# Kernel tuning notes

Hardware: AMD Instinct MI355X
Metric: run time of the kernel (lower is better)

The kernel has to match this reference:

```python
import jax, jax.numpy as jnp
import numpy as np

B, S, NB = 2, 1024, 64
V, D, L, H, F = 1024, 512, 12, 8, 2048
DH = D // H
MAX_BARS = 256


def _ln(x, g, b):
    m = x.mean(-1, keepdims=True)
    v = ((x - m) ** 2).mean(-1, keepdims=True)
    return (x - m) * jax.lax.rsqrt(v + 1e-5) * g + b


def _rope(x, pos):
    # x: (B, T, H, DH), pos: (T,)
    half = x.shape[-1] // 2
    inv = 10000.0 ** (-jnp.arange(half, dtype=jnp.float32) / half)
    f = pos.astype(jnp.float32)[:, None] * inv  # (T, half)
    cos = jnp.cos(f)[None, :, None, :]
    sin = jnp.sin(f)[None, :, None, :]
    x1, x2 = x[..., :half], x[..., half:]
    return jnp.concatenate([x1 * cos - x2 * sin, x1 * sin + x2 * cos], -1)


def _swiglu(h, w1, w3, w2):
    return (jax.nn.silu(h @ w1) * (h @ w3)) @ w2


def _attention(sum_x, x, Wq, Wk, Wv, Wo, smask, umask, pos_s, pos_r):
    # shared QKV/O projections over both streams; 4-way block mask via concat keys
    b, nb, _ = sum_x.shape
    s = x.shape[1]

    def proj(t, W):
        return (t @ W).reshape(t.shape[0], t.shape[1], H, DH)

    qs = _rope(proj(sum_x, Wq), pos_s)
    qr = _rope(proj(x, Wq), pos_r)
    k = jnp.concatenate([_rope(proj(sum_x, Wk), pos_s), _rope(proj(x, Wk), pos_r)], 1)
    v = jnp.concatenate([proj(sum_x, Wv), proj(x, Wv)], 1)
    scale = DH ** -0.5

    def attend(q, mask):
        sc = jnp.einsum('bqhd,bkhd->bhqk', q, k) * scale
        sc = jnp.where(mask[:, None], sc, -1e9)
        p = jax.nn.softmax(sc, axis=-1)
        o = jnp.einsum('bhqk,bkhd->bqhd', p, v)
        return o.reshape(q.shape[0], q.shape[1], D)

    return attend(qs, smask) @ Wo, attend(qr, umask) @ Wo


def _forward(tok_emb, inst_emb, bar_emb,
             ln_as_g, ln_as_b, ln_ar_g, ln_ar_b,
             ln_fs_g, ln_fs_b, ln_fr_g, ln_fr_b,
             Wq, Wk, Wv, Wo,
             fs_w1, fs_w3, fs_w2, fr_w1, fr_w3, fr_w2,
             out_g, out_b,
             token_ids, chord_ids, instrument_ids, num_bars):
    b, s = token_ids.shape
    nb = num_bars
    x = tok_emb[token_ids] + inst_emb[jnp.clip(instrument_ids, 0, 129)]
    sum_x = jnp.broadcast_to(bar_emb[:nb][None], (b, nb, tok_emb.shape[1]))

    bars = jnp.arange(nb)
    idx = jnp.arange(s)
    # ss: summary b attends summaries b' <= b (causal over bars)
    ss = jnp.broadcast_to(jnp.tril(jnp.ones((nb, nb), bool))[None], (b, nb, nb))
    # sr: summary b summarizes regular tokens in bar b
    sr = chord_ids[:, None, :] == bars[None, :, None]  # (B, nb, S)
    smask = jnp.concatenate([ss, sr], -1)  # (B, nb, nb+S)
    # rs: regular i attends summaries of strictly previous bars
    rs = bars[None, None, :] < chord_ids[:, :, None]  # (B, S, nb)
    # rr: regular i attends regular j in same bar, causally
    rr = (chord_ids[:, :, None] == chord_ids[:, None, :]) & (idx[:, None] >= idx[None, :])
    umask = jnp.concatenate([rs, rr], -1)  # (B, S, nb+S)

    pos_s = jnp.arange(nb)
    pos_r = jnp.arange(s)

    for l in range(Wq.shape[0]):
        a_s, a_r = _attention(_ln(sum_x, ln_as_g[l], ln_as_b[l]),
                              _ln(x, ln_ar_g[l], ln_ar_b[l]),
                              Wq[l], Wk[l], Wv[l], Wo[l], smask, umask, pos_s, pos_r)
        sum_x = sum_x + a_s
        x = x + a_r
        sum_x = sum_x + _swiglu(_ln(sum_x, ln_fs_g[l], ln_fs_b[l]), fs_w1[l], fs_w3[l], fs_w2[l])
        x = x + _swiglu(_ln(x, ln_fr_g[l], ln_fr_b[l]), fr_w1[l], fr_w3[l], fr_w2[l])

    x = _ln(x, out_g, out_b)
    return x @ tok_emb.T  # tied lm_head


def setup_inputs():
    key = jax.random.key(0)
    it = iter(jax.random.split(key, 40))

    def nrm(shape):
        return jax.random.normal(next(it), shape, jnp.float32) * 0.02

    inp = {
        'token_ids': jax.random.randint(next(it), (B, S), 0, V),
        'chord_ids': jnp.sort(jax.random.randint(next(it), (B, S), 0, NB), axis=-1),
        'instrument_ids': jax.random.randint(next(it), (B, S), 0, 130),
        'num_bars': NB,
        'tok_emb': nrm((V, D)),
        'inst_emb': nrm((130, D)),
        'bar_emb': nrm((MAX_BARS, D)),
        'ln_as_g': jnp.ones((L, D)), 'ln_as_b': jnp.zeros((L, D)),
        'ln_ar_g': jnp.ones((L, D)), 'ln_ar_b': jnp.zeros((L, D)),
        'ln_fs_g': jnp.ones((L, D)), 'ln_fs_b': jnp.zeros((L, D)),
        'ln_fr_g': jnp.ones((L, D)), 'ln_fr_b': jnp.zeros((L, D)),
        'Wq': nrm((L, D, D)), 'Wk': nrm((L, D, D)),
        'Wv': nrm((L, D, D)), 'Wo': nrm((L, D, D)),
        'fs_w1': nrm((L, D, F)), 'fs_w3': nrm((L, D, F)), 'fs_w2': nrm((L, F, D)),
        'fr_w1': nrm((L, D, F)), 'fr_w3': nrm((L, D, F)), 'fr_w2': nrm((L, F, D)),
        'out_g': jnp.ones((D,)), 'out_b': jnp.zeros((D,)),
    }
    return inp


def reference(token_ids, chord_ids, instrument_ids, num_bars,
              tok_emb, inst_emb, bar_emb,
              ln_as_g, ln_as_b, ln_ar_g, ln_ar_b,
              ln_fs_g, ln_fs_b, ln_fr_g, ln_fr_b,
              Wq, Wk, Wv, Wo,
              fs_w1, fs_w3, fs_w2, fr_w1, fr_w3, fr_w2,
              out_g, out_b):
    return _forward(tok_emb, inst_emb, bar_emb,
                    ln_as_g, ln_as_b, ln_ar_g, ln_ar_b,
                    ln_fs_g, ln_fs_b, ln_fr_g, ln_fr_b,
                    Wq, Wk, Wv, Wo,
                    fs_w1, fs_w3, fs_w2, fr_w1, fr_w3, fr_w2,
                    out_g, out_b,
                    token_ids, chord_ids, instrument_ids, num_bars)
```

## Files before the change

### kernel.cpp

```cpp
#include <hip/hip_runtime.h>
#include <stdint.h>

#define NB 64
#define BATCH 2
#define SEQ 1024
#define DMODEL 512
#define NHEAD 8
#define DHEAD 64
#define FDIM 2048
#define NLAYER 12
#define VOCAB 1024
#define KTOT (NB + SEQ)
#define RSUM (BATCH * NB)
#define RREG (BATCH * SEQ)
#define RTOT (RSUM + RREG)

using bf16x8 = __attribute__((ext_vector_type(8))) short;
using f32x4  = __attribute__((ext_vector_type(4))) float;

__device__ __forceinline__ unsigned short f2bf(float f) {
  union { float f; unsigned u; } c; c.f = f;
  return (unsigned short)((c.u + 0x7fffu + ((c.u >> 16) & 1u)) >> 16);
}
__device__ __forceinline__ float bf2f(unsigned short s) {
  union { unsigned u; float f; } c; c.u = ((unsigned)s) << 16;
  return c.f;
}

template<int R>
__device__ __forceinline__ void stage_tile(
    const unsigned short* __restrict__ G, int K, int base_row, int k0,
    unsigned short (*lds)[64], int wid, int lane)
{
  const int rl = lane >> 3;
  const int j  = lane & 7;
  #pragma unroll
  for (int c = 0; c < R / 32; ++c) {
    const int r0 = wid * (R / 4) + c * 8;
    const int row = r0 + rl;
    const unsigned short* g = G + (size_t)(base_row + row) * K + k0
                                + ((j ^ (row & 7)) << 3);
    __builtin_amdgcn_global_load_lds(
        (const __attribute__((address_space(1))) void*)g,
        (__attribute__((address_space(3))) void*)&lds[r0][0], 16, 0, 0);
  }
}

__device__ __forceinline__ bf16x8 lds_frag(const unsigned short (*lds)[64],
                                           int row, int cc) {
  return *(const bf16x8*)&lds[row][(cc ^ (row & 7)) << 3];
}

template<int BM, int BN, int EPI>
__global__ __launch_bounds__(256) void gemm_bt(
    const unsigned short* __restrict__ A, const unsigned short* __restrict__ B0,
    const unsigned short* __restrict__ B1,
    void* __restrict__ Cout, const float* resid, int N, int K)
{
  constexpr int BK = 64;
  constexpr int WM = BM / 2, WN = BN / 2;
  constexpr int FM = WM / 16, FN = WN / 16;
  __shared__ __align__(16) unsigned short As[BM][BK];
  __shared__ __align__(16) unsigned short Bs[BN][BK];
  const int bm = blockIdx.y * BM, bn = blockIdx.x * BN;
  const unsigned short* __restrict__ BT = (bm < RSUM) ? B0 : B1;
  const int tid = threadIdx.x;
  const int wid = tid >> 6, lane = tid & 63;
  const int wm = wid >> 1, wn = wid & 1;
  const int lr = lane & 15, lk = lane >> 4;
  f32x4 acc[FM][FN] = {};
  for (int k0 = 0; k0 < K; k0 += BK) {
    __syncthreads();
    stage_tile<BM>(A,  K, bm, k0, As, wid, lane);
    stage_tile<BN>(BT, K, bn, k0, Bs, wid, lane);
    __syncthreads();
    #pragma unroll
    for (int kk = 0; kk < 2; ++kk) {
      bf16x8 af[FM], bfr[FN];
      #pragma unroll
      for (int m = 0; m < FM; ++m)
        af[m] = lds_frag(As, wm * WM + m * 16 + lr, kk * 4 + lk);
      #pragma unroll
      for (int n = 0; n < FN; ++n)
        bfr[n] = lds_frag(Bs, wn * WN + n * 16 + lr, kk * 4 + lk);
      #pragma unroll
      for (int m = 0; m < FM; ++m)
        #pragma unroll
        for (int n = 0; n < FN; ++n)
          acc[m][n] = __builtin_amdgcn_mfma_f32_16x16x32_bf16(af[m], bfr[n], acc[m][n], 0, 0, 0);
    }
  }
  #pragma unroll
  for (int m = 0; m < FM; ++m)
    #pragma unroll
    for (int n = 0; n < FN; ++n)
      #pragma unroll
      for (int i = 0; i < 4; ++i) {
        int row = bm + wm * WM + m * 16 + lk * 4 + i;
        int col = bn + wn * WN + n * 16 + lr;
        float v = acc[m][n][i];
        if constexpr (EPI == 1) {
          const float other = __shfl_xor(v, 1, 64);
          if (!(lr & 1)) {
            const float g = v, u = other;
            const float hv = (g / (1.f + __expf(-g))) * u;
            unsigned short* C = (unsigned short*)Cout;
            C[(size_t)row * (N >> 1) + (col >> 1)] = f2bf(hv);
          }
        } else if constexpr (EPI == 2) {
          unsigned short* C = (unsigned short*)Cout;
          C[(size_t)row * N + col] = f2bf(v);
        } else {
          float* C = (float*)Cout;
          size_t idx = (size_t)row * N + col;
          if (resid) v += resid[idx];
          C[idx] = v;
        }
      }
}

__global__ __launch_bounds__(256) void transpose_conv_kernel(
    const float* __restrict__ src, unsigned short* __restrict__ dst,
    int K, int N, size_t sstride, size_t dstride, int rmul, int radd)
{
  __shared__ float tile[32][33];
  const float* s = src + (size_t)blockIdx.z * sstride;
  unsigned short* d = dst + (size_t)blockIdx.z * dstride;
  const int k0 = blockIdx.y * 32, n0 = blockIdx.x * 32;
  const int tx = threadIdx.x & 31, ty = threadIdx.x >> 5;
  #pragma unroll
  for (int i = 0; i < 32; i += 8)
    tile[ty + i][tx] = s[(size_t)(k0 + ty + i) * N + n0 + tx];
  __syncthreads();
  #pragma unroll
  for (int i = 0; i < 32; i += 8)
    d[((size_t)(n0 + ty + i) * rmul + radd) * K + k0 + tx] = f2bf(tile[tx][ty + i]);
}

__global__ __launch_bounds__(256) void convert_bf16_kernel(
    const float* __restrict__ src, unsigned short* __restrict__ dst)
{
  const int i = (blockIdx.x * 256 + threadIdx.x) * 4;
  const float4 v = *(const float4*)&src[i];
  union { unsigned short u[4]; uint2 q; } o;
  o.u[0] = f2bf(v.x); o.u[1] = f2bf(v.y); o.u[2] = f2bf(v.z); o.u[3] = f2bf(v.w);
  *(uint2*)&dst[i] = o.q;
}

__global__ __launch_bounds__(128) void embed_kernel(
    const int* __restrict__ tok, const int* __restrict__ inst,
    const float* __restrict__ tok_emb, const float* __restrict__ inst_emb,
    const float* __restrict__ bar_emb, float* __restrict__ z)
{
  const int r = blockIdx.x, t = threadIdx.x;
  float4 val;
  if (r < RSUM) {
    const int bar = r & (NB - 1);
    val = *(const float4*)&bar_emb[(size_t)bar * DMODEL + t * 4];
  } else {
    const int rr = r - RSUM;
    const int b = rr >> 10, i = rr & (SEQ - 1);
    const int tk = tok[b * SEQ + i];
    int ins = inst[b * SEQ + i];
    ins = ins < 0 ? 0 : (ins > 129 ? 129 : ins);
    const float4 a = *(const float4*)&tok_emb[(size_t)tk * DMODEL + t * 4];
    const float4 cc = *(const float4*)&inst_emb[(size_t)ins * DMODEL + t * 4];
    val.x = a.x + cc.x; val.y = a.y + cc.y; val.z = a.z + cc.z; val.w = a.w + cc.w;
  }
  *(float4*)&z[(size_t)r * DMODEL + t * 4] = val;
}

__global__ __launch_bounds__(256) void ln_dual_kernel(
    const float* __restrict__ x, const float* __restrict__ g_s,
    const float* __restrict__ b_s, const float* __restrict__ g_r,
    const float* __restrict__ b_r, unsigned short* __restrict__ out)
{
  const int wid = threadIdx.x >> 6, lane = threadIdx.x & 63;
  const size_t row = (size_t)blockIdx.x * 4 + wid;
  const float* g = (row < RSUM) ? g_s : g_r;
  const float* bb = (row < RSUM) ? b_s : b_r;
  const float* xr = x + row * DMODEL + lane * 8;
  float v[8];
  *(float4*)&v[0] = *(const float4*)&xr[0];
  *(float4*)&v[4] = *(const float4*)&xr[4];
  float s = 0.f;
  #pragma unroll
  for (int j = 0; j < 8; ++j) s += v[j];
  #pragma unroll
  for (int o = 32; o > 0; o >>= 1) s += __shfl_xor(s, o, 64);
  const float mean = s * (1.f / DMODEL);
  float vs = 0.f;
  #pragma unroll
  for (int j = 0; j < 8; ++j) { float d = v[j] - mean; vs += d * d; }
  #pragma unroll
  for (int o = 32; o > 0; o >>= 1) vs += __shfl_xor(vs, o, 64);
  const float rs = rsqrtf(vs * (1.f / DMODEL) + 1e-5f);
  float gg[8], bv[8];
  *(float4*)&gg[0] = *(const float4*)&g[lane * 8];
  *(float4*)&gg[4] = *(const float4*)&g[lane * 8 + 4];
  *(float4*)&bv[0] = *(const float4*)&bb[lane * 8];
  *(float4*)&bv[4] = *(const float4*)&bb[lane * 8 + 4];
  union { unsigned short u[8]; uint4 q; } o8;
  #pragma unroll
  for (int j = 0; j < 8; ++j) o8.u[j] = f2bf((v[j] - mean) * rs * gg[j] + bv[j]);
  *(uint4*)&out[row * DMODEL + lane * 8] = o8.q;
}

__global__ __launch_bounds__(256) void ln_kernel(
    const float* __restrict__ x, const float* __restrict__ g,
    const float* __restrict__ bb, unsigned short* __restrict__ out)
{
  const int wid = threadIdx.x >> 6, lane = threadIdx.x & 63;
  const size_t row = (size_t)blockIdx.x * 4 + wid;
  const float* xr = x + row * DMODEL + lane * 8;
  float v[8];
  *(float4*)&v[0] = *(const float4*)&xr[0];
  *(float4*)&v[4] = *(const float4*)&xr[4];
  float s = 0.f;
  #pragma unroll
  for (int j = 0; j < 8; ++j) s += v[j];
  #pragma unroll
  for (int o = 32; o > 0; o >>= 1) s += __shfl_xor(s, o, 64);
  const float mean = s * (1.f / DMODEL);
  float vs = 0.f;
  #pragma unroll
  for (int j = 0; j < 8; ++j) { float d = v[j] - mean; vs += d * d; }
  #pragma unroll
  for (int o = 32; o > 0; o >>= 1) vs += __shfl_xor(vs, o, 64);
  const float rs = rsqrtf(vs * (1.f / DMODEL) + 1e-5f);
  float gg[8], bv[8];
  *(float4*)&gg[0] = *(const float4*)&g[lane * 8];
  *(float4*)&gg[4] = *(const float4*)&g[lane * 8 + 4];
  *(float4*)&bv[0] = *(const float4*)&bb[lane * 8];
  *(float4*)&bv[4] = *(const float4*)&bb[lane * 8 + 4];
  union { unsigned short u[8]; uint4 q; } o8;
  #pragma unroll
  for (int j = 0; j < 8; ++j) o8.u[j] = f2bf((v[j] - mean) * rs * gg[j] + bv[j]);
  *(uint4*)&out[row * DMODEL + lane * 8] = o8.q;
}

__global__ void rope_table_kernel(float* __restrict__ cost, float* __restrict__ sint) {
  const int pos = blockIdx.x, j = threadIdx.x;
  const float inv = powf(10000.f, -(float)j / 32.f);
  const float f = (float)pos * inv;
  cost[pos * 32 + j] = cosf(f);
  sint[pos * 32 + j] = sinf(f);
}

__global__ void segstart_kernel(const int* __restrict__ chord, int* __restrict__ seg) {
  const int b = blockIdx.x, t = threadIdx.x;
  if (t <= NB) {
    int lo = 0, hi = SEQ;
    while (lo < hi) {
      int mid = (lo + hi) >> 1;
      if (chord[b * SEQ + mid] < t) lo = mid + 1; else hi = mid;
    }
    seg[b * (NB + 1) + t] = lo;
  }
}

__global__ __launch_bounds__(256) void rope_scatter_kernel(
    const unsigned short* __restrict__ qkv, const float* __restrict__ cost,
    const float* __restrict__ sint, unsigned short* __restrict__ q_cat,
    unsigned short* __restrict__ k_cat, unsigned short* __restrict__ v_cat)
{
  const int r = blockIdx.x, tid = threadIdx.x;
  int b, pos, catrow;
  if (r < RSUM) { b = r >> 6; pos = r & (NB - 1); catrow = pos; }
  else { const int rr = r - RSUM; b = rr >> 10; pos = rr & (SEQ - 1); catrow = NB + pos; }
  const unsigned short* src = qkv + (size_t)r * (3 * DMODEL);
  const int d = tid & 63;
  const int j = d & 31;
  const float cs = cost[pos * 32 + j];
  const float sn = sint[pos * 32 + j];
  #pragma unroll
  for (int hh = 0; hh < 2; ++hh) {
    const int h = (tid >> 6) + hh * 4;
    const float xq = bf2f(src[h * 64 + d]),          xq2 = bf2f(src[h * 64 + (d ^ 32)]);
    const float xk = bf2f(src[DMODEL + h * 64 + d]), xk2 = bf2f(src[DMODEL + h * 64 + (d ^ 32)]);
    const unsigned short vv = src[2 * DMODEL + h * 64 + d];
    const float qv = (d < 32) ? (xq * cs - xq2 * sn) : (xq2 * sn + xq * cs);
    const float kv = (d < 32) ? (xk * cs - xk2 * sn) : (xk2 * sn + xk * cs);
    const size_t base = ((size_t)(b * NHEAD + h) * KTOT + catrow) * DHEAD + d;
    q_cat[base] = f2bf(qv); k_cat[base] = f2bf(kv); v_cat[base] = vv;
  }
}

__global__ __launch_bounds__(256) void attn_kernel(
    const unsigned short* __restrict__ q_cat, const unsigned short* __restrict__ k_cat,
    const unsigned short* __restrict__ v_cat, const int* __restrict__ seg,
    const int* __restrict__ chord, unsigned short* __restrict__ att)
{
  const int h = blockIdx.y, b = blockIdx.z;
  const int wid = threadIdx.x >> 6, lane = threadIdx.x & 63;
  const int qi = blockIdx.x * 4 + wid;
  int qrow, nsum, s0, nk, outrow;
  if (qi < NB) {
    const int c = qi;
    s0 = seg[b * (NB + 1) + c];
    const int s1 = seg[b * (NB + 1) + c + 1];
    qrow = c; nsum = c + 1; nk = nsum + (s1 - s0);
    outrow = b * NB + c;
  } else {
    const int i = qi - NB;
    const int c = chord[b * SEQ + i];
    s0 = seg[b * (NB + 1) + c];
    qrow = NB + i; nsum = c; nk = nsum + (i - s0 + 1);
    outrow = RSUM + b * SEQ + i;
  }
  const size_t bh = (size_t)(b * NHEAD + h) * KTOT * DHEAD;
  const unsigned short* __restrict__ Kp = k_cat + bh;
  const unsigned short* __restrict__ Vp = v_cat + bh;
  __shared__ __align__(16) float qsh[4][DHEAD];
  __shared__ __align__(16) float psh[4][64];
  qsh[wid][lane] = bf2f(q_cat[bh + (size_t)qrow * DHEAD + lane]) * 0.125f;
  const int lq = lane & 3;
  const int lkey = lane >> 2;
  float m = -1e30f, l = 0.f, o = 0.f;
  for (int t0 = 0; t0 < nk; t0 += 64) {
    float sv[4];
    float tmax = -3.0e38f;
    #pragma unroll
    for (int pass = 0; pass < 4; ++pass) {
      const int t = t0 + pass * 16 + lkey;
      int kr = (t < nsum) ? t : (NB + s0 + (t - nsum));
      if (kr > KTOT - 1) kr = KTOT - 1;
      const bf16x8* krp = (const bf16x8*)(Kp + (size_t)kr * DHEAD + lq * 16);
      const bf16x8 k0v = krp[0], k1v = krp[1];
      float a = 0.f;
      #pragma unroll
      for (int dd = 0; dd < 8; ++dd)
        a = fmaf(qsh[wid][lq * 16 + dd], bf2f((unsigned short)k0v[dd]), a);
      #pragma unroll
      for (int dd = 0; dd < 8; ++dd)
        a = fmaf(qsh[wid][lq * 16 + 8 + dd], bf2f((unsigned short)k1v[dd]), a);
      a += __shfl_xor(a, 1, 64);
      a += __shfl_xor(a, 2, 64);
      sv[pass] = (t < nk) ? a : -3.0e38f;
      tmax = fmaxf(tmax, sv[pass]);
    }
    #pragma unroll
    for (int off = 32; off > 0; off >>= 1) tmax = fmaxf(tmax, __shfl_xor(tmax, off, 64));
    const float mn = fmaxf(m, tmax);
    float psum = 0.f;
    #pragma unroll
    for (int pass = 0; pass < 4; ++pass) {
      const float pp = __expf(sv[pass] - mn);
      psum += pp;
      if (lq == 0) psh[wid][pass * 16 + lkey] = pp;
    }
    psum *= 0.25f;
    #pragma unroll
    for (int off = 32; off > 0; off >>= 1) psum += __shfl_xor(psum, off, 64);
    const float scale = __expf(m - mn);
    l = l * scale + psum;
    o *= scale;
    m = mn;
    const int rem = nk - t0;
    const int kn = rem < 64 ? rem : 64;
    for (int k = 0; k < kn; k += 4) {
      const float4 pv = *(const float4*)&psh[wid][k];
      const float pj[4] = {pv.x, pv.y, pv.z, pv.w};
      #pragma unroll
      for (int j = 0; j < 4; ++j) {
        const int tk = t0 + k + j;
        int kr = (tk < nsum) ? tk : (NB + s0 + (tk - nsum));
        if (kr > KTOT - 1) kr = KTOT - 1;
        o = fmaf(pj[j], bf2f(Vp[(size_t)kr * DHEAD + lane]), o);
      }
    }
  }
  att[(size_t)outrow * DMODEL + h * DHEAD + lane] = f2bf(o / l);
}

extern "C" void kernel_launch(void* const* d_in, const int* in_sizes, int n_in,
                              void* d_out, int out_size, void* d_ws, size_t ws_size,
                              hipStream_t stream)
{
  const int* tok      = (const int*)d_in[0];
  const int* chord    = (const int*)d_in[1];
  const int* inst     = (const int*)d_in[2];
  const float* tok_emb  = (const float*)d_in[4];
  const float* inst_emb = (const float*)d_in[5];
  const float* bar_emb  = (const float*)d_in[6];
  const float* ln_as_g = (const float*)d_in[7];
  const float* ln_as_b = (const float*)d_in[8];
  const float* ln_ar_g = (const float*)d_in[9];
  const float* ln_ar_b = (const float*)d_in[10];
  const float* ln_fs_g = (const float*)d_in[11];
  const float* ln_fs_b = (const float*)d_in[12];
  const float* ln_fr_g = (const float*)d_in[13];
  const float* ln_fr_b = (const float*)d_in[14];
  const float* Wq = (const float*)d_in[15];
  const float* Wk = (const float*)d_in[16];
  const float* Wv = (const float*)d_in[17];
  const float* Wo = (const float*)d_in[18];
  const float* fs_w1 = (const float*)d_in[19];
  const float* fs_w3 = (const float*)d_in[20];
  const float* fs_w2 = (const float*)d_in[21];
  const float* fr_w1 = (const float*)d_in[22];
  const float* fr_w3 = (const float*)d_in[23];
  const float* fr_w2 = (const float*)d_in[24];
  const float* out_g = (const float*)d_in[25];
  const float* out_b = (const float*)d_in[26];

  char* p = (char*)d_ws;
  auto alloc = [&](size_t bytes) -> void* {
    void* r = (void*)p;
    p += (bytes + 255) & ~(size_t)255;
    return r;
  };
  unsigned short* WqkvT  = (unsigned short*)alloc((size_t)NLAYER * 1536 * 512 * 2);
  unsigned short* WoT    = (unsigned short*)alloc((size_t)NLAYER * 512 * 512 * 2);
  unsigned short* fsW13T = (unsigned short*)alloc((size_t)NLAYER * 4096 * 512 * 2);
  unsigned short* frW13T = (unsigned short*)alloc((size_t)NLAYER * 4096 * 512 * 2);
  unsigned short* fsW2T  = (unsigned short*)alloc((size_t)NLAYER * 512 * 2048 * 2);
  unsigned short* frW2T  = (unsigned short*)alloc((size_t)NLAYER * 512 * 2048 * 2);
  unsigned short* tokT   = (unsigned short*)alloc((size_t)VOCAB * DMODEL * 2);
  float* z           = (float*)alloc((size_t)RTOT * DMODEL * 4);
  unsigned short* zn = (unsigned short*)alloc((size_t)RTOT * DMODEL * 2);
  unsigned short* qkv = (unsigned short*)alloc((size_t)RTOT * 3 * DMODEL * 2);
  unsigned short* q_cat = (unsigned short*)alloc((size_t)BATCH * NHEAD * KTOT * DHEAD * 2);
  unsigned short* k_cat = (unsigned short*)alloc((size_t)BATCH * NHEAD * KTOT * DHEAD * 2);
  unsigned short* v_cat = (unsigned short*)alloc((size_t)BATCH * NHEAD * KTOT * DHEAD * 2);
  unsigned short* att = (unsigned short*)alloc((size_t)RTOT * DMODEL * 2);
  unsigned short* h1 = (unsigned short*)alloc((size_t)RTOT * FDIM * 2);
  float* cost        = (float*)alloc((size_t)SEQ * 32 * 4);
  float* sint        = (float*)alloc((size_t)SEQ * 32 * 4);
  int* seg           = (int*)alloc((size_t)BATCH * (NB + 1) * 4);
  if ((size_t)(p - (char*)d_ws) > ws_size) return;

  transpose_conv_kernel<<<dim3(16, 16, NLAYER), 256, 0, stream>>>(Wq, WqkvT,                    512, 512,  (size_t)512*512,  (size_t)1536*512, 1, 0);
  transpose_conv_kernel<<<dim3(16, 16, NLAYER), 256, 0, stream>>>(Wk, WqkvT + (size_t)512*512,  512, 512,  (size_t)512*512,  (size_t)1536*512, 1, 0);
  transpose_conv_kernel<<<dim3(16, 16, NLAYER), 256, 0, stream>>>(Wv, WqkvT + (size_t)1024*512, 512, 512,  (size_t)512*512,  (size_t)1536*512, 1, 0);
  transpose_conv_kernel<<<dim3(16, 16, NLAYER), 256, 0, stream>>>(Wo, WoT,                      512, 512,  (size_t)512*512,  (size_t)512*512,  1, 0);
  transpose_conv_kernel<<<dim3(64, 16, NLAYER), 256, 0, stream>>>(fs_w1, fsW13T, 512, 2048, (size_t)512*2048, (size_t)4096*512, 2, 0);
  transpose_conv_kernel<<<dim3(64, 16, NLAYER), 256, 0, stream>>>(fs_w3, fsW13T, 512, 2048, (size_t)512*2048, (size_t)4096*512, 2, 1);
  transpose_conv_kernel<<<dim3(64, 16, NLAYER), 256, 0, stream>>>(fr_w1, frW13T, 512, 2048, (size_t)512*2048, (size_t)4096*512, 2, 0);
  transpose_conv_kernel<<<dim3(64, 16, NLAYER), 256, 0, stream>>>(fr_w3, frW13T, 512, 2048, (size_t)512*2048, (size_t)4096*512, 2, 1);
  transpose_conv_kernel<<<dim3(16, 64, NLAYER), 256, 0, stream>>>(fs_w2, fsW2T, 2048, 512, (size_t)2048*512, (size_t)512*2048, 1, 0);
  transpose_conv_kernel<<<dim3(16, 64, NLAYER), 256, 0, stream>>>(fr_w2, frW2T, 2048, 512, (size_t)2048*512, (size_t)512*2048, 1, 0);
  convert_bf16_kernel<<<VOCAB * DMODEL / 1024, 256, 0, stream>>>(tok_emb, tokT);

  embed_kernel<<<RTOT, 128, 0, stream>>>(tok, inst, tok_emb, inst_emb, bar_emb, z);
  rope_table_kernel<<<SEQ, 32, 0, stream>>>(cost, sint);
  segstart_kernel<<<BATCH, 128, 0, stream>>>(chord, seg);

  for (int l = 0; l < NLAYER; ++l) {
    const size_t ld = (size_t)l * DMODEL;
    ln_dual_kernel<<<RTOT / 4, 256, 0, stream>>>(z, ln_as_g + ld, ln_as_b + ld,
                                                 ln_ar_g + ld, ln_ar_b + ld, zn);
    gemm_bt<64, 64, 2><<<dim3(1536 / 64, RTOT / 64), 256, 0, stream>>>(
        zn, WqkvT + (size_t)l * 1536 * 512, WqkvT + (size_t)l * 1536 * 512,
        qkv, nullptr, 1536, 512);
    rope_scatter_kernel<<<RTOT, 256, 0, stream>>>(qkv, cost, sint, q_cat, k_cat, v_cat);
    attn_kernel<<<dim3(KTOT / 4, NHEAD, BATCH), 256, 0, stream>>>(q_cat, k_cat, v_cat, seg, chord, att);
    gemm_bt<64, 32, 0><<<dim3(512 / 32, RTOT / 64), 256, 0, stream>>>(
        att, WoT + (size_t)l * 512 * 512, WoT + (size_t)l * 512 * 512,
        z, z, 512, 512);
    ln_dual_kernel<<<RTOT / 4, 256, 0, stream>>>(z, ln_fs_g + ld, ln_fs_b + ld,
                                                 ln_fr_g + ld, ln_fr_b + ld, zn);
    gemm_bt<64, 64, 1><<<dim3(4096 / 64, RTOT / 64), 256, 0, stream>>>(
        zn, fsW13T + (size_t)l * 4096 * 512, frW13T + (size_t)l * 4096 * 512,
        h1, nullptr, 4096, 512);
    gemm_bt<64, 32, 0><<<dim3(512 / 32, RTOT / 64), 256, 0, stream>>>(
        h1, fsW2T + (size_t)l * 512 * 2048, frW2T + (size_t)l * 512 * 2048,
        z, z, 512, 2048);
  }

  ln_kernel<<<RREG / 4, 256, 0, stream>>>(z + (size_t)RSUM * DMODEL, out_g, out_b,
                                          zn + (size_t)RSUM * DMODEL);
  gemm_bt<64, 64, 0><<<dim3(VOCAB / 64, RREG / 64), 256, 0, stream>>>(
      zn + (size_t)RSUM * DMODEL, tokT, tokT, (float*)d_out, nullptr, VOCAB, 512);
}
```

Before: 1.426 ms.

## Fuse RoPE and head scatter into QKV GEMM epilogue; vectorize attention PV loop

The QKV GEMM gains an epilogue mode that stages the accumulator tile in shared memory, applies RoPE to the Q and K columns and writes bf16 rows directly into the per-head q/k/v concatenated buffers. This removes the intermediate qkv buffer and the separate rope_scatter kernel launch. The attention kernel's PV accumulation now has each lane load 4 contiguous V elements for a quarter of the keys, then reduces across lane groups with shuffles. This replaces per-lane scalar V loads with wider loads and adds shuffle reductions plus extra shared memory in the GEMM epilogue.

```diff
diff --git a/kernel.cpp b/kernel.cpp
--- a/kernel.cpp
+++ b/kernel.cpp
@@ -16,6 +16,7 @@
 #define RTOT (RSUM + RREG)
 
 using bf16x8 = __attribute__((ext_vector_type(8))) short;
+using bf16x4 = __attribute__((ext_vector_type(4))) short;
 using f32x4  = __attribute__((ext_vector_type(4))) float;
 
 __device__ __forceinline__ unsigned short f2bf(float f) {
@@ -55,13 +56,19 @@
 __global__ __launch_bounds__(256) void gemm_bt(
     const unsigned short* __restrict__ A, const unsigned short* __restrict__ B0,
     const unsigned short* __restrict__ B1,
-    void* __restrict__ Cout, const float* resid, int N, int K)
+    void* __restrict__ Cout, const float* resid, int N, int K,
+    const float* __restrict__ cost, const float* __restrict__ sint,
+    unsigned short* __restrict__ kcat, unsigned short* __restrict__ vcat)
 {
   constexpr int BK = 64;
   constexpr int WM = BM / 2, WN = BN / 2;
   constexpr int FM = WM / 16, FN = WN / 16;
-  __shared__ __align__(16) unsigned short As[BM][BK];
-  __shared__ __align__(16) unsigned short Bs[BN][BK];
+  constexpr int SM_STAGE = (BM + BN) * BK * 2;
+  constexpr int SM_CT = (EPI == 3) ? 64 * 66 * 4 : 0;
+  constexpr int SMSZ = SM_STAGE > SM_CT ? SM_STAGE : SM_CT;
+  __shared__ __align__(16) unsigned char smem[SMSZ];
+  auto As = (unsigned short (*)[BK])smem;
+  auto Bs = (unsigned short (*)[BK])(smem + BM * BK * 2);
   const int bm = blockIdx.y * BM, bn = blockIdx.x * BN;
   const unsigned short* __restrict__ BT = (bm < RSUM) ? B0 : B1;
   const int tid = threadIdx.x;
@@ -89,6 +96,47 @@
         for (int n = 0; n < FN; ++n)
           acc[m][n] = __builtin_amdgcn_mfma_f32_16x16x32_bf16(af[m], bfr[n], acc[m][n], 0, 0, 0);
     }
+  }
+  if constexpr (EPI == 3) {
+    __syncthreads();
+    auto ct = (float (*)[66])smem;
+    #pragma unroll
+    for (int m = 0; m < FM; ++m)
+      #pragma unroll
+      for (int n = 0; n < FN; ++n)
+        #pragma unroll
+        for (int i = 0; i < 4; ++i)
+          ct[wm * WM + m * 16 + lk * 4 + i][wn * WN + n * 16 + lr] = acc[m][n][i];
+    __syncthreads();
+    const int r = tid >> 2, quad = tid & 3;
+    const int tr = bm + r;
+    int b, pos, catrow;
+    if (tr < RSUM) { b = tr >> 6; pos = tr & (NB - 1); catrow = pos; }
+    else { const int rr = tr - RSUM; b = rr >> 10; pos = rr & (SEQ - 1); catrow = NB + pos; }
+    const int part = bn >> 9;
+    const int head = (bn & 511) >> 6;
+    const size_t obase = ((size_t)(b * NHEAD + head) * KTOT + catrow) * DHEAD + quad * 16;
+    union { unsigned short u[16]; uint4 q[2]; } ob;
+    if (part == 2) {
+      #pragma unroll
+      for (int j = 0; j < 16; ++j) ob.u[j] = f2bf(ct[r][quad * 16 + j]);
+      *(uint4*)&vcat[obase] = ob.q[0];
+      *(uint4*)&vcat[obase + 8] = ob.q[1];
+    } else {
+      #pragma unroll
+      for (int j = 0; j < 16; ++j) {
+        const int d = quad * 16 + j;
+        const float v = ct[r][d];
+        const float other = ct[r][d ^ 32];
+        const float cs = cost[pos * 32 + (d & 31)];
+        const float sn = sint[pos * 32 + (d & 31)];
+        ob.u[j] = f2bf((d < 32) ? (v * cs - other * sn) : (other * sn + v * cs));
+      }
+      unsigned short* dst = part ? kcat : (unsigned short*)Cout;
+      *(uint4*)&dst[obase] = ob.q[0];
+      *(uint4*)&dst[obase + 8] = ob.q[1];
+    }
+    return;
   }
   #pragma unroll
   for (int m = 0; m < FM; ++m)
@@ -259,33 +307,6 @@
   }
 }
 
-__global__ __launch_bounds__(256) void rope_scatter_kernel(
-    const unsigned short* __restrict__ qkv, const float* __restrict__ cost,
-    const float* __restrict__ sint, unsigned short* __restrict__ q_cat,
-    unsigned short* __restrict__ k_cat, unsigned short* __restrict__ v_cat)
-{
-  const int r = blockIdx.x, tid = threadIdx.x;
-  int b, pos, catrow;
-  if (r < RSUM) { b = r >> 6; pos = r & (NB - 1); catrow = pos; }
-  else { const int rr = r - RSUM; b = rr >> 10; pos = rr & (SEQ - 1); catrow = NB + pos; }
-  const unsigned short* src = qkv + (size_t)r * (3 * DMODEL);
-  const int d = tid & 63;
-  const int j = d & 31;
-  const float cs = cost[pos * 32 + j];
-  const float sn = sint[pos * 32 + j];
-  #pragma unroll
-  for (int hh = 0; hh < 2; ++hh) {
-    const int h = (tid >> 6) + hh * 4;
-    const float xq = bf2f(src[h * 64 + d]),          xq2 = bf2f(src[h * 64 + (d ^ 32)]);
-    const float xk = bf2f(src[DMODEL + h * 64 + d]), xk2 = bf2f(src[DMODEL + h * 64 + (d ^ 32)]);
-    const unsigned short vv = src[2 * DMODEL + h * 64 + d];
-    const float qv = (d < 32) ? (xq * cs - xq2 * sn) : (xq2 * sn + xq * cs);
-    const float kv = (d < 32) ? (xk * cs - xk2 * sn) : (xk2 * sn + xk * cs);
-    const size_t base = ((size_t)(b * NHEAD + h) * KTOT + catrow) * DHEAD + d;
-    q_cat[base] = f2bf(qv); k_cat[base] = f2bf(kv); v_cat[base] = vv;
-  }
-}
-
 __global__ __launch_bounds__(256) void attn_kernel(
     const unsigned short* __restrict__ q_cat, const unsigned short* __restrict__ k_cat,
     const unsigned short* __restrict__ v_cat, const int* __restrict__ seg,
@@ -316,7 +337,10 @@
   qsh[wid][lane] = bf2f(q_cat[bh + (size_t)qrow * DHEAD + lane]) * 0.125f;
   const int lq = lane & 3;
   const int lkey = lane >> 2;
-  float m = -1e30f, l = 0.f, o = 0.f;
+  const int kk = lane >> 4;
+  const int dd = lane & 15;
+  float m = -1e30f, l = 0.f;
+  float4 o4 = {0.f, 0.f, 0.f, 0.f};
   for (int t0 = 0; t0 < nk; t0 += 64) {
     float sv[4];
     float tmax = -3.0e38f;
@@ -329,11 +353,11 @@
       const bf16x8 k0v = krp[0], k1v = krp[1];
       float a = 0.f;
       #pragma unroll
-      for (int dd = 0; dd < 8; ++dd)
-        a = fmaf(qsh[wid][lq * 16 + dd], bf2f((unsigned short)k0v[dd]), a);
-      #pragma unroll
-      for (int dd = 0; dd < 8; ++dd)
-        a = fmaf(qsh[wid][lq * 16 + 8 + dd], bf2f((unsigned short)k1v[dd]), a);
+      for (int d2 = 0; d2 < 8; ++d2)
+        a = fmaf(qsh[wid][lq * 16 + d2], bf2f((unsigned short)k0v[d2]), a);
+      #pragma unroll
+      for (int d2 = 0; d2 < 8; ++d2)
+        a = fmaf(qsh[wid][lq * 16 + 8 + d2], bf2f((unsigned short)k1v[d2]), a);
       a += __shfl_xor(a, 1, 64);
       a += __shfl_xor(a, 2, 64);
       sv[pass] = (t < nk) ? a : -3.0e38f;
@@ -354,23 +378,36 @@
     for (int off = 32; off > 0; off >>= 1) psum += __shfl_xor(psum, off, 64);
     const float scale = __expf(m - mn);
     l = l * scale + psum;
-    o *= scale;
+    o4.x *= scale; o4.y *= scale; o4.z *= scale; o4.w *= scale;
     m = mn;
-    const int rem = nk - t0;
-    const int kn = rem < 64 ? rem : 64;
-    for (int k = 0; k < kn; k += 4) {
-      const float4 pv = *(const float4*)&psh[wid][k];
-      const float pj[4] = {pv.x, pv.y, pv.z, pv.w};
-      #pragma unroll
-      for (int j = 0; j < 4; ++j) {
-        const int tk = t0 + k + j;
-        int kr = (tk < nsum) ? tk : (NB + s0 + (tk - nsum));
-        if (kr > KTOT - 1) kr = KTOT - 1;
-        o = fmaf(pj[j], bf2f(Vp[(size_t)kr * DHEAD + lane]), o);
-      }
+    #pragma unroll
+    for (int j = 0; j < 16; ++j) {
+      const int toff = j * 4 + kk;
+      const float p = psh[wid][toff];
+      const int tk = t0 + toff;
+      int kr = (tk < nsum) ? tk : (NB + s0 + (tk - nsum));
+      if (kr > KTOT - 1) kr = KTOT - 1;
+      const bf16x4 vv = *(const bf16x4*)&Vp[(size_t)kr * DHEAD + dd * 4];
+      o4.x = fmaf(p, bf2f((unsigned short)vv[0]), o4.x);
+      o4.y = fmaf(p, bf2f((unsigned short)vv[1]), o4.y);
+      o4.z = fmaf(p, bf2f((unsigned short)vv[2]), o4.z);
+      o4.w = fmaf(p, bf2f((unsigned short)vv[3]), o4.w);
     }
   }
-  att[(size_t)outrow * DMODEL + h * DHEAD + lane] = f2bf(o / l);
+  #pragma unroll
+  for (int off = 16; off <= 32; off <<= 1) {
+    o4.x += __shfl_xor(o4.x, off, 64);
+    o4.y += __shfl_xor(o4.y, off, 64);
+    o4.z += __shfl_xor(o4.z, off, 64);
+    o4.w += __shfl_xor(o4.w, off, 64);
+  }
+  if (kk == 0) {
+    const float invl = 1.f / l;
+    union { unsigned short u[4]; uint2 q; } ob;
+    ob.u[0] = f2bf(o4.x * invl); ob.u[1] = f2bf(o4.y * invl);
+    ob.u[2] = f2bf(o4.z * invl); ob.u[3] = f2bf(o4.w * invl);
+    *(uint2*)&att[(size_t)outrow * DMODEL + h * DHEAD + dd * 4] = ob.q;
+  }
 }
 
 extern "C" void kernel_launch(void* const* d_in, const int* in_sizes, int n_in,
@@ -419,7 +456,6 @@
   unsigned short* tokT   = (unsigned short*)alloc((size_t)VOCAB * DMODEL * 2);
   float* z           = (float*)alloc((size_t)RTOT * DMODEL * 4);
   unsigned short* zn = (unsigned short*)alloc((size_t)RTOT * DMODEL * 2);
-  unsigned short* qkv = (unsigned short*)alloc((size_t)RTOT * 3 * DMODEL * 2);
   unsigned short* q_cat = (unsigned short*)alloc((size_t)BATCH * NHEAD * KTOT * DHEAD * 2);
   unsigned short* k_cat = (unsigned short*)alloc((size_t)BATCH * NHEAD * KTOT * DHEAD * 2);
   unsigned short* v_cat = (unsigned short*)alloc((size_t)BATCH * NHEAD * KTOT * DHEAD * 2);
@@ -450,26 +486,26 @@
     const size_t ld = (size_t)l * DMODEL;
     ln_dual_kernel<<<RTOT / 4, 256, 0, stream>>>(z, ln_as_g + ld, ln_as_b + ld,
                                                  ln_ar_g + ld, ln_ar_b + ld, zn);
-    gemm_bt<64, 64, 2><<<dim3(1536 / 64, RTOT / 64), 256, 0, stream>>>(
+    gemm_bt<64, 64, 3><<<dim3(1536 / 64, RTOT / 64), 256, 0, stream>>>(
         zn, WqkvT + (size_t)l * 1536 * 512, WqkvT + (size_t)l * 1536 * 512,
-        qkv, nullptr, 1536, 512);
-    rope_scatter_kernel<<<RTOT, 256, 0, stream>>>(qkv, cost, sint, q_cat, k_cat, v_cat);
+        q_cat, nullptr, 1536, 512, cost, sint, k_cat, v_cat);
     attn_kernel<<<dim3(KTOT / 4, NHEAD, BATCH), 256, 0, stream>>>(q_cat, k_cat, v_cat, seg, chord, att);
     gemm_bt<64, 32, 0><<<dim3(512 / 32, RTOT / 64), 256, 0, stream>>>(
         att, WoT + (size_t)l * 512 * 512, WoT + (size_t)l * 512 * 512,
-        z, z, 512, 512);
+        z, z, 512, 512, nullptr, nullptr, nullptr, nullptr);
     ln_dual_kernel<<<RTOT / 4, 256, 0, stream>>>(z, ln_fs_g + ld, ln_fs_b + ld,
                                                  ln_fr_g + ld, ln_fr_b + ld, zn);
     gemm_bt<64, 64, 1><<<dim3(4096 / 64, RTOT / 64), 256, 0, stream>>>(
         zn, fsW13T + (size_t)l * 4096 * 512, frW13T + (size_t)l * 4096 * 512,
-        h1, nullptr, 4096, 512);
+        h1, nullptr, 4096, 512, nullptr, nullptr, nullptr, nullptr);
     gemm_bt<64, 32, 0><<<dim3(512 / 32, RTOT / 64), 256, 0, stream>>>(
         h1, fsW2T + (size_t)l * 512 * 2048, frW2T + (size_t)l * 512 * 2048,
-        z, z, 512, 2048);
+        z, z, 512, 2048, nullptr, nullptr, nullptr, nullptr);
   }
 
   ln_kernel<<<RREG / 4, 256, 0, stream>>>(z + (size_t)RSUM * DMODEL, out_g, out_b,
                                           zn + (size_t)RSUM * DMODEL);
   gemm_bt<64, 64, 0><<<dim3(VOCAB / 64, RREG / 64), 256, 0, stream>>>(
-      zn + (size_t)RSUM * DMODEL, tokT, tokT, (float*)d_out, nullptr, VOCAB, 512);
-}
+      zn + (size_t)RSUM * DMODEL, tokT, tokT, (float*)d_out, nullptr, VOCAB, 512,
+      nullptr, nullptr, nullptr, nullptr);
+}
```

New measurement: 1.320 ms. 7.5% less time.
